# Optimization experiments

Measured on AMD Instinct MI355X. Metric: run time of the kernel, lower is better.

Reference implementation:

```python
import jax, jax.numpy as jnp
import numpy as np

PREVIOUS_VISIT = 64


def setup_inputs() -> dict:
    key = jax.random.key(0)
    k1, k2, k3, k4 = jax.random.split(key, 4)
    B, T, D, H = 1024, 64, 512, 512
    scale = 1.0 / np.sqrt(D)
    return {
        "input_context": jax.random.normal(k1, (B, T, D), dtype=jnp.float32),
        "kernel": jax.random.normal(k2, (D, 4 * H), dtype=jnp.float32) * scale,
        "recurrent_kernel": jax.random.normal(k3, (H, 4 * H), dtype=jnp.float32) * scale,
        "bias": jax.random.normal(k4, (4 * H,), dtype=jnp.float32) * 0.01,
    }


def reference(input_context, kernel, recurrent_kernel, bias):
    # Keras LSTMCell unrolled over PREVIOUS_VISIT steps; gate order i, f, c, o.
    B = input_context.shape[0]
    H = recurrent_kernel.shape[0]
    xs = jnp.transpose(input_context[:, :PREVIOUS_VISIT, :], (1, 0, 2))  # [T, B, D]

    def step(carry, xt):
        h, c = carry
        z = xt @ kernel + h @ recurrent_kernel + bias  # [B, 4H]
        i, f, g, o = jnp.split(z, 4, axis=-1)
        i = jax.nn.sigmoid(i)
        f = jax.nn.sigmoid(f)
        g = jnp.tanh(g)
        o = jax.nn.sigmoid(o)
        c_new = f * c + i * g
        h_new = o * jnp.tanh(c_new)
        return (h_new, c_new), h_new

    init = (jnp.zeros((B, H), dtype=input_context.dtype),
            jnp.zeros((B, H), dtype=input_context.dtype))
    _, hs = jax.lax.scan(step, init, xs)  # hs: [T, B, H]
    return jnp.transpose(hs, (1, 0, 2))  # [B, T, H]
```

## Files before the change

kernel.cpp:

```cpp
#include <hip/hip_runtime.h>
#include <hip/hip_bf16.h>
#include <hip/hip_fp16.h>


typedef __attribute__((ext_vector_type(8))) short bfrag8;
typedef __attribute__((ext_vector_type(4))) float facc4;
typedef __attribute__((ext_vector_type(4))) unsigned int u32x4;

#define MFMA_B16(a, b, c) __builtin_amdgcn_mfma_f32_16x16x32_bf16(a, b, c, 0, 0, 0)

#define GRP 16u

__device__ __forceinline__ unsigned short f2bf(float f) {
  unsigned int u = __float_as_uint(f);
  u += 0x7FFFu + ((u >> 16) & 1u);
  return (unsigned short)(u >> 16);
}
__device__ __forceinline__ float sigm(float x)  { return 1.0f / (1.0f + __expf(-x)); }
__device__ __forceinline__ float tanh_(float x) { return 1.0f - 2.0f / (__expf(2.0f * x) + 1.0f); }

__device__ __forceinline__ void gl2lds16(const void* g, void* l) {
  __builtin_amdgcn_global_load_lds(
      (const __attribute__((address_space(1))) unsigned int*)g,
      (__attribute__((address_space(3))) unsigned int*)l, 16, 0, 0);
}

__device__ __forceinline__ u32x4 ld128_coh(const void* p) {
  u32x4 r;
  asm volatile("global_load_dwordx4 %0, %1, off sc0 sc1" : "=v"(r) : "v"(p));
  return r;
}
__device__ __forceinline__ void st128_coh(void* p, u32x4 v) {
  asm volatile("global_store_dwordx4 %0, %1, off sc0 sc1" :: "v"(p), "v"(v));
}

__device__ __forceinline__ int foff(int row, int seg) {
  return (row << 7) + ((((seg & 8) | ((seg ^ row) & 7))) << 3);
}

__device__ __forceinline__ void group_barrier(unsigned int* bar, int slot) {
  asm volatile("s_waitcnt vmcnt(0)" ::: "memory");
  __syncthreads();
  if (threadIdx.x == 0) {
    __hip_atomic_fetch_add(&bar[slot], 1u, __ATOMIC_RELAXED, __HIP_MEMORY_SCOPE_AGENT);
    while (__hip_atomic_load(&bar[slot], __ATOMIC_RELAXED, __HIP_MEMORY_SCOPE_AGENT) < GRP)
      __builtin_amdgcn_s_sleep(2);
  }
  __syncthreads();
}


__global__ void prep_w(const float* __restrict__ Wk, const float* __restrict__ Wr,
                       const float* __restrict__ bias,
                       unsigned short* __restrict__ Wx, unsigned short* __restrict__ Wh,
                       float* __restrict__ biasr, unsigned int* __restrict__ bar)
{
  int gid = (blockIdx.x << 8) + threadIdx.x;
  int k   = gid >> 11;
  int col = gid & 2047;
  float v = (k < 512) ? Wk[((size_t)k << 11) + col]
                      : Wr[((size_t)(k - 512) << 11) + col];
  int n = ((col & 511) << 2) | (col >> 9);
  if (k < 512) Wx[((size_t)n << 9) + k]         = f2bf(v);
  else         Wh[((size_t)n << 9) + (k - 512)] = f2bf(v);
  if (gid < 2048) biasr[((gid & 511) << 2) | (gid >> 9)] = bias[gid];
  if (gid < 1024) bar[gid] = 0u;
}

__global__ void prep_x(const float* __restrict__ x, unsigned short* __restrict__ Xbf)
{
  int flat = (blockIdx.x << 8) + threadIdx.x;
  int d8 = flat & 63;
  int b  = (flat >> 6) & 1023;
  int t  = flat >> 16;
  const float* src = x + ((((size_t)b << 6) + t) << 9) + (d8 << 3);
  float4 v0 = *(const float4*)src;
  float4 v1 = *(const float4*)(src + 4);
  uint4 u;
  u.x = f2bf(v0.x) | ((unsigned)f2bf(v0.y) << 16);
  u.y = f2bf(v0.z) | ((unsigned)f2bf(v0.w) << 16);
  u.z = f2bf(v1.x) | ((unsigned)f2bf(v1.y) << 16);
  u.w = f2bf(v1.z) | ((unsigned)f2bf(v1.w) << 16);
  *(uint4*)&Xbf[((((size_t)t << 10) + b) << 9) + (d8 << 3)] = u;
}

__global__ __launch_bounds__(256, 3)
void zx_gemm(const unsigned short* __restrict__ Xbf, const unsigned short* __restrict__ Wx,
             unsigned short* __restrict__ zx)
{
  __shared__ __align__(16) unsigned short As[8192];
  __shared__ __align__(16) unsigned short Bs[8192];
  __shared__ float Zs[64][68];

  const int tid  = threadIdx.x;
  const int lane = tid & 63;
  const int w    = tid >> 6;
  const int llo  = lane & 15;
  const int lhi  = lane >> 4;
  const int wm   = (w >> 1) & 1;
  const int wn   = w & 1;

  const int n0 = blockIdx.x << 6;
  const int by = blockIdx.y;
  const int t  = by >> 4;
  const int b0 = (by & 15) << 6;

  facc4 acc00 = {0.f,0.f,0.f,0.f};
  facc4 acc01 = acc00, acc10 = acc00, acc11 = acc00;

  const int am0 = (wm << 5) + llo;
  const int bn0 = (wn << 5) + llo;

  for (int ci = 0; ci < 4; ++ci) {
    const int kb = ci << 7;
#pragma unroll
    for (int j = 0; j < 4; ++j) {
      int p = (j << 8) + tid;
      int r = p >> 4, ps = p & 15;
      int s = (ps & 8) | ((ps ^ r) & 7);
      gl2lds16(Xbf + ((((size_t)t << 10) + (b0 + r)) << 9) + kb + (s << 3), &As[p << 3]);
      gl2lds16(Wx  + (((size_t)(n0 + r)) << 9) + kb + (s << 3),             &Bs[p << 3]);
    }
    __syncthreads();
#pragma unroll
    for (int kk = 0; kk < 4; ++kk) {
      const int s0 = (kk << 2) + lhi;
      bfrag8 a0 = *(const bfrag8*)&As[foff(am0,      s0)];
      bfrag8 a1 = *(const bfrag8*)&As[foff(am0 + 16, s0)];
      bfrag8 b0 = *(const bfrag8*)&Bs[foff(bn0,      s0)];
      bfrag8 b1 = *(const bfrag8*)&Bs[foff(bn0 + 16, s0)];
      acc00 = MFMA_B16(a0, b0, acc00);
      acc01 = MFMA_B16(a0, b1, acc01);
      acc10 = MFMA_B16(a1, b0, acc10);
      acc11 = MFMA_B16(a1, b1, acc11);
    }
    __syncthreads();
  }

#pragma unroll
  for (int rr = 0; rr < 4; ++rr) {
    int rbase = (wm << 5) + (lhi << 2) + rr;
    int cbase = (wn << 5) + llo;
    Zs[rbase][cbase]           = acc00[rr];
    Zs[rbase][cbase + 16]      = acc01[rr];
    Zs[rbase + 16][cbase]      = acc10[rr];
    Zs[rbase + 16][cbase + 16] = acc11[rr];
  }
  __syncthreads();

  const int hs = tid & 15;
  const int rw = tid >> 4;
#pragma unroll
  for (int it = 0; it < 4; ++it) {
    int row = rw + (it << 4);
    float4 z = *(const float4*)&Zs[row][hs << 2];
    ushort4 o;
    o.x = __half_as_ushort(__float2half(z.x));
    o.y = __half_as_ushort(__float2half(z.y));
    o.z = __half_as_ushort(__float2half(z.z));
    o.w = __half_as_ushort(__float2half(z.w));
    *(ushort4*)&zx[((((size_t)t << 10) + (b0 + row)) << 11) + n0 + (hs << 2)] = o;
  }
}

__global__ __launch_bounds__(256, 1)
void lstm_persist(unsigned short* __restrict__ Hbuf,
                  const unsigned short* __restrict__ Wh,
                  const unsigned short* __restrict__ zx,
                  const float* __restrict__ biasr,
                  float* __restrict__ out,
                  unsigned int* __restrict__ bar)
{
  extern __shared__ __align__(16) char smem_raw[];
  unsigned short* Bs = (unsigned short*)smem_raw;
  unsigned short* As = (unsigned short*)(smem_raw + 131072);
  unsigned short* Sc = (unsigned short*)(smem_raw + 147456);

  const int tid  = threadIdx.x;
  const int lane = tid & 63;
  const int w    = tid >> 6;
  const int llo  = lane & 15;
  const int lhi  = lane >> 4;

  const int bx  = blockIdx.x;
  const int nbI = bx & 15;
  const int mg  = bx >> 4;
  const int m0  = mg << 6;
  const int n0  = nbI << 7;
  const int hb  = nbI << 5;

  for (int i = 0; i < 32; ++i) {
    int p  = (i << 8) + tid;
    int ci = p >> 11;
    int q  = p & 2047;
    int r  = q >> 4, ps = q & 15;
    int s  = (ps & 8) | ((ps ^ r) & 7);
    gl2lds16(Wh + (((size_t)(n0 + r)) << 9) + (ci << 7) + (s << 3), Bs + ((size_t)p << 3));
  }

  const int nw0 = w << 5;
  float4 bb[2];
  bb[0] = *(const float4*)&biasr[(size_t)(hb + (w << 3) + 0 + lhi) << 2];
  bb[1] = *(const float4*)&biasr[(size_t)(hb + (w << 3) + 4 + lhi) << 2];

  float c[2][4] = {{0.f,0.f,0.f,0.f},{0.f,0.f,0.f,0.f}};

  asm volatile("s_waitcnt vmcnt(0)" ::: "memory");
  __syncthreads();

  const size_t HSTG = (size_t)16 * 1024 * 32;

  for (int t = 0; t < 64; ++t) {
    const unsigned short* zxt = zx + ((size_t)t << 21);

    ushort4 zp[2][4];
#pragma unroll
    for (int nt = 0; nt < 2; ++nt)
#pragma unroll
      for (int bt = 0; bt < 4; ++bt) {
        int b = m0 + (bt << 4) + llo;
        int h = hb + (w << 3) + (nt << 2) + lhi;
        zp[nt][bt] = *(const ushort4*)&zxt[((size_t)b << 11) + (h << 2)];
      }

    if (t) group_barrier(bar, ((t - 1) << 4) + mg);

    facc4 acc[2][4];
#pragma unroll
    for (int nt = 0; nt < 2; ++nt)
#pragma unroll
      for (int bt = 0; bt < 4; ++bt)
        acc[nt][bt] = (facc4){0.f, 0.f, 0.f, 0.f};

    if (t) {
      const unsigned short* Hs = Hbuf + (size_t)(t & 1) * HSTG;
      u32x4 av[16];
#pragma unroll
      for (int ci = 0; ci < 4; ++ci)
#pragma unroll
        for (int j = 0; j < 4; ++j) {
          int p = (j << 8) + tid;
          int r = p >> 4, ps = p & 15;
          int s = (ps & 8) | ((ps ^ r) & 7);
          int nbp = (ci << 2) + (s >> 2);
          av[(ci << 2) + j] =
              ld128_coh(Hs + ((size_t)nbp << 15) + ((size_t)(m0 + r) << 5) + ((s & 3) << 3));
        }
#pragma unroll
      for (int ci = 0; ci < 4; ++ci) {
        if      (ci == 0) asm volatile("s_waitcnt vmcnt(12)" ::: "memory");
        else if (ci == 1) asm volatile("s_waitcnt vmcnt(8)"  ::: "memory");
        else if (ci == 2) asm volatile("s_waitcnt vmcnt(4)"  ::: "memory");
        else              asm volatile("s_waitcnt vmcnt(0)"  ::: "memory");
        __builtin_amdgcn_sched_barrier(0);
#pragma unroll
        for (int j = 0; j < 4; ++j) {
          int p = (j << 8) + tid;
          *(u32x4*)&As[(size_t)p << 3] = av[(ci << 2) + j];
        }
        __syncthreads();
#pragma unroll
        for (int kk = 0; kk < 4; ++kk) {
          const int s0 = (kk << 2) + lhi;
          bfrag8 wh0 = *(const bfrag8*)&Bs[(ci << 14) + foff(nw0 + llo,      s0)];
          bfrag8 wh1 = *(const bfrag8*)&Bs[(ci << 14) + foff(nw0 + 16 + llo, s0)];
#pragma unroll
          for (int bt = 0; bt < 4; ++bt) {
            bfrag8 hf = *(const bfrag8*)&As[foff((bt << 4) + llo, s0)];
            acc[0][bt] = MFMA_B16(wh0, hf, acc[0][bt]);
            acc[1][bt] = MFMA_B16(wh1, hf, acc[1][bt]);
          }
        }
        __syncthreads();
      }
    }

#pragma unroll
    for (int nt = 0; nt < 2; ++nt)
#pragma unroll
      for (int bt = 0; bt < 4; ++bt) {
        int b = m0 + (bt << 4) + llo;
        int h = hb + (w << 3) + (nt << 2) + lhi;
        float zi = acc[nt][bt][0] + __half2float(__ushort_as_half(zp[nt][bt].x)) + bb[nt].x;
        float zf = acc[nt][bt][1] + __half2float(__ushort_as_half(zp[nt][bt].y)) + bb[nt].y;
        float zg = acc[nt][bt][2] + __half2float(__ushort_as_half(zp[nt][bt].z)) + bb[nt].z;
        float zo = acc[nt][bt][3] + __half2float(__ushort_as_half(zp[nt][bt].w)) + bb[nt].w;
        float ig = sigm(zi);
        float fg = sigm(zf);
        float gg = tanh_(zg);
        float og = sigm(zo);
        float cn = fg * c[nt][bt] + ig * gg;
        c[nt][bt] = cn;
        float hn = og * tanh_(cn);
        Sc[(w << 9) + (((bt << 4) + llo) << 3) + (nt << 2) + lhi] = f2bf(hn);
        out[((size_t)b << 15) + ((size_t)t << 9) + h] = hn;
      }
    __syncthreads();
    {
      u32x4 hv = *(const u32x4*)&Sc[((tid & 3) << 9) + ((tid >> 2) << 3)];
      unsigned short* Hn = Hbuf + (size_t)((t + 1) & 1) * HSTG;
      st128_coh(Hn + ((size_t)nbI << 15) + ((size_t)(m0 + (tid >> 2)) << 5) + ((tid & 3) << 3), hv);
    }
  }
}

extern "C" void kernel_launch(void* const* d_in, const int* in_sizes, int n_in,
                              void* d_out, int out_size, void* d_ws, size_t ws_size,
                              hipStream_t stream) {
  const float* x    = (const float*)d_in[0];
  const float* Wk   = (const float*)d_in[1];
  const float* Wr   = (const float*)d_in[2];
  const float* bias = (const float*)d_in[3];
  float* out = (float*)d_out;

  char* ws = (char*)d_ws;
  unsigned short* Wx    = (unsigned short*)(ws);
  unsigned short* Wh    = (unsigned short*)(ws + (2u << 20));
  float*          biasr = (float*)(ws + (4u << 20));
  unsigned short* Hbuf  = (unsigned short*)(ws + (4u << 20) + 8192);
  unsigned int*   bar   = (unsigned int*)(ws + (6u << 20) + 8192);
  unsigned short* Xbf   = (unsigned short*)(ws + (8u << 20) + 8192);
  unsigned short* zx    = (unsigned short*)(ws + (72u << 20) + 8192);

  (void)hipFuncSetAttribute((const void*)lstm_persist,
                            hipFuncAttributeMaxDynamicSharedMemorySize, 151552);

  prep_w<<<dim3(8192), dim3(256), 0, stream>>>(Wk, Wr, bias, Wx, Wh, biasr, bar);
  prep_x<<<dim3(16384), dim3(256), 0, stream>>>(x, Xbf);
  zx_gemm<<<dim3(32, 1024), dim3(256), 0, stream>>>(Xbf, Wx, zx);
  lstm_persist<<<dim3(256), dim3(256), 151552, stream>>>(Hbuf, Wh, zx, biasr, out, bar);
}
```

Before: 1.376 ms.

## Replace group barrier with per-chunk readiness counters and quad-buffered hidden state

The full 16-block group barrier is replaced by fine-grained counters: each block signals after its hidden-state store lands, and consumers wait only on four counters, one per K-chunk group of four producer blocks. The hidden-state ring grows from two to four buffers so producers can run ahead without overwriting data still being read. The output store is moved after the H publish and excluded from the wait via vmcnt(8), so the signal does not wait on output writes. This cuts idle time at step boundaries, at the cost of more workspace and a subtler memory-ordering argument (relaxed atomics, relying on vmcnt ordering).

Result: faster. 1.164 ms (-15.4%).

```diff
diff --git a/kernel.cpp b/kernel.cpp
--- a/kernel.cpp
+++ b/kernel.cpp
@@ -8,8 +8,6 @@
 typedef __attribute__((ext_vector_type(4))) unsigned int u32x4;
 
 #define MFMA_B16(a, b, c) __builtin_amdgcn_mfma_f32_16x16x32_bf16(a, b, c, 0, 0, 0)
-
-#define GRP 16u
 
 __device__ __forceinline__ unsigned short f2bf(float f) {
   unsigned int u = __float_as_uint(f);
@@ -31,29 +29,18 @@
   return r;
 }
 __device__ __forceinline__ void st128_coh(void* p, u32x4 v) {
-  asm volatile("global_store_dwordx4 %0, %1, off sc0 sc1" :: "v"(p), "v"(v));
+  asm volatile("global_store_dwordx4 %0, %1, off sc0 sc1" :: "v"(p), "v"(v) : "memory");
 }
 
 __device__ __forceinline__ int foff(int row, int seg) {
   return (row << 7) + ((((seg & 8) | ((seg ^ row) & 7))) << 3);
-}
-
-__device__ __forceinline__ void group_barrier(unsigned int* bar, int slot) {
-  asm volatile("s_waitcnt vmcnt(0)" ::: "memory");
-  __syncthreads();
-  if (threadIdx.x == 0) {
-    __hip_atomic_fetch_add(&bar[slot], 1u, __ATOMIC_RELAXED, __HIP_MEMORY_SCOPE_AGENT);
-    while (__hip_atomic_load(&bar[slot], __ATOMIC_RELAXED, __HIP_MEMORY_SCOPE_AGENT) < GRP)
-      __builtin_amdgcn_s_sleep(2);
-  }
-  __syncthreads();
 }
 
 
 __global__ void prep_w(const float* __restrict__ Wk, const float* __restrict__ Wr,
                        const float* __restrict__ bias,
                        unsigned short* __restrict__ Wx, unsigned short* __restrict__ Wh,
-                       float* __restrict__ biasr, unsigned int* __restrict__ bar)
+                       float* __restrict__ biasr, unsigned int* __restrict__ cnt)
 {
   int gid = (blockIdx.x << 8) + threadIdx.x;
   int k   = gid >> 11;
@@ -64,7 +51,7 @@
   if (k < 512) Wx[((size_t)n << 9) + k]         = f2bf(v);
   else         Wh[((size_t)n << 9) + (k - 512)] = f2bf(v);
   if (gid < 2048) biasr[((gid & 511) << 2) | (gid >> 9)] = bias[gid];
-  if (gid < 1024) bar[gid] = 0u;
+  if (gid < 4096) cnt[gid] = 0u;
 }
 
 __global__ void prep_x(const float* __restrict__ x, unsigned short* __restrict__ Xbf)
@@ -169,7 +156,7 @@
                   const unsigned short* __restrict__ zx,
                   const float* __restrict__ biasr,
                   float* __restrict__ out,
-                  unsigned int* __restrict__ bar)
+                  unsigned int* __restrict__ cnt)
 {
   extern __shared__ __align__(16) char smem_raw[];
   unsigned short* Bs = (unsigned short*)smem_raw;
@@ -223,8 +210,6 @@
         zp[nt][bt] = *(const ushort4*)&zxt[((size_t)b << 11) + (h << 2)];
       }
 
-    if (t) group_barrier(bar, ((t - 1) << 4) + mg);
-
     facc4 acc[2][4];
 #pragma unroll
     for (int nt = 0; nt < 2; ++nt)
@@ -233,7 +218,14 @@
         acc[nt][bt] = (facc4){0.f, 0.f, 0.f, 0.f};
 
     if (t) {
-      const unsigned short* Hs = Hbuf + (size_t)(t & 1) * HSTG;
+      if (tid < 4) {
+        const unsigned int* cp = cnt + (t << 6) + (mg << 2) + tid;
+        while (__hip_atomic_load(cp, __ATOMIC_RELAXED, __HIP_MEMORY_SCOPE_AGENT) < 4u)
+          __builtin_amdgcn_s_sleep(1);
+      }
+      __syncthreads();
+
+      const unsigned short* Hs = Hbuf + (size_t)(t & 3) * HSTG;
       u32x4 av[16];
 #pragma unroll
       for (int ci = 0; ci < 4; ++ci)
@@ -275,12 +267,11 @@
       }
     }
 
+    float hn_s[2][4];
 #pragma unroll
     for (int nt = 0; nt < 2; ++nt)
 #pragma unroll
       for (int bt = 0; bt < 4; ++bt) {
-        int b = m0 + (bt << 4) + llo;
-        int h = hb + (w << 3) + (nt << 2) + lhi;
         float zi = acc[nt][bt][0] + __half2float(__ushort_as_half(zp[nt][bt].x)) + bb[nt].x;
         float zf = acc[nt][bt][1] + __half2float(__ushort_as_half(zp[nt][bt].y)) + bb[nt].y;
         float zg = acc[nt][bt][2] + __half2float(__ushort_as_half(zp[nt][bt].z)) + bb[nt].z;
@@ -292,14 +283,31 @@
         float cn = fg * c[nt][bt] + ig * gg;
         c[nt][bt] = cn;
         float hn = og * tanh_(cn);
+        hn_s[nt][bt] = hn;
         Sc[(w << 9) + (((bt << 4) + llo) << 3) + (nt << 2) + lhi] = f2bf(hn);
-        out[((size_t)b << 15) + ((size_t)t << 9) + h] = hn;
       }
     __syncthreads();
-    {
+
+    if (t < 63) {
       u32x4 hv = *(const u32x4*)&Sc[((tid & 3) << 9) + ((tid >> 2) << 3)];
-      unsigned short* Hn = Hbuf + (size_t)((t + 1) & 1) * HSTG;
+      unsigned short* Hn = Hbuf + (size_t)((t + 1) & 3) * HSTG;
       st128_coh(Hn + ((size_t)nbI << 15) + ((size_t)(m0 + (tid >> 2)) << 5) + ((tid & 3) << 3), hv);
+    }
+#pragma unroll
+    for (int nt = 0; nt < 2; ++nt)
+#pragma unroll
+      for (int bt = 0; bt < 4; ++bt) {
+        int b = m0 + (bt << 4) + llo;
+        int h = hb + (w << 3) + (nt << 2) + lhi;
+        out[((size_t)b << 15) + ((size_t)t << 9) + h] = hn_s[nt][bt];
+      }
+    if (t < 63) {
+      if (t == 0) asm volatile("s_waitcnt vmcnt(0)" ::: "memory");
+      else        asm volatile("s_waitcnt vmcnt(8)" ::: "memory");
+      __syncthreads();
+      if (tid == 0)
+        __hip_atomic_fetch_add(&cnt[((t + 1) << 6) + (mg << 2) + (nbI >> 2)], 1u,
+                               __ATOMIC_RELAXED, __HIP_MEMORY_SCOPE_AGENT);
     }
   }
 }
@@ -317,16 +325,16 @@
   unsigned short* Wx    = (unsigned short*)(ws);
   unsigned short* Wh    = (unsigned short*)(ws + (2u << 20));
   float*          biasr = (float*)(ws + (4u << 20));
-  unsigned short* Hbuf  = (unsigned short*)(ws + (4u << 20) + 8192);
-  unsigned int*   bar   = (unsigned int*)(ws + (6u << 20) + 8192);
-  unsigned short* Xbf   = (unsigned short*)(ws + (8u << 20) + 8192);
-  unsigned short* zx    = (unsigned short*)(ws + (72u << 20) + 8192);
+  unsigned int*   cnt   = (unsigned int*)(ws + (4u << 20) + 8192);
+  unsigned short* Hbuf  = (unsigned short*)(ws + (5u << 20));
+  unsigned short* Xbf   = (unsigned short*)(ws + (9u << 20));
+  unsigned short* zx    = (unsigned short*)(ws + (73u << 20));
 
   (void)hipFuncSetAttribute((const void*)lstm_persist,
                             hipFuncAttributeMaxDynamicSharedMemorySize, 151552);
 
-  prep_w<<<dim3(8192), dim3(256), 0, stream>>>(Wk, Wr, bias, Wx, Wh, biasr, bar);
+  prep_w<<<dim3(8192), dim3(256), 0, stream>>>(Wk, Wr, bias, Wx, Wh, biasr, cnt);
   prep_x<<<dim3(16384), dim3(256), 0, stream>>>(x, Xbf);
   zx_gemm<<<dim3(32, 1024), dim3(256), 0, stream>>>(Xbf, Wx, zx);
-  lstm_persist<<<dim3(256), dim3(256), 151552, stream>>>(Hbuf, Wh, zx, biasr, out, bar);
-}
+  lstm_persist<<<dim3(256), dim3(256), 151552, stream>>>(Hbuf, Wh, zx, biasr, out, cnt);
+}
```
